# Optimization experiments

Hardware: AMD Instinct MI355X
Metric: run time of the kernel (lower is better)

Reference implementation:

```python
import jax, jax.numpy as jnp
import numpy as np

E = 8      # num_experts
K = 2      # top-k
DIM = 1024
DFF = 2048  # fused gate+up width; intermediate = DFF // 2 == DIM


def setup_inputs() -> dict:
    key = jax.random.key(0)
    ks = jax.random.split(key, 5)
    B, S = 4, 2048
    x = jax.random.normal(ks[0], (B, S, DIM), dtype=jnp.float32)
    Wg = jax.random.normal(ks[1], (E, DIM), dtype=jnp.float32) * 0.02
    bg = jax.random.normal(ks[2], (E,), dtype=jnp.float32) * 0.02
    w1 = jax.random.normal(ks[3], (E, DFF, DIM), dtype=jnp.float32) * 0.02
    w2 = jax.random.normal(ks[4], (E, DIM, DFF // 2), dtype=jnp.float32) * 0.02
    return {"x": x, "Wg": Wg, "bg": bg, "w1": w1, "w2": w2}


def _moe(x, Wg, bg, w1, w2):
    B, S, D = x.shape
    t = x.reshape(-1, D)                      # [T, D] tokens
    logits = t @ Wg.T + bg                    # [T, E]
    probs = jax.nn.softmax(logits, axis=-1)
    topw, topi = jax.lax.top_k(probs, K)      # [T, K]
    topw = topw / jnp.sum(topw, axis=-1, keepdims=True)  # renormalize=True
    # per-token combine weight for each expert (0 if not selected): [T, E]
    combine = jnp.sum(jax.nn.one_hot(topi, E, dtype=t.dtype) * topw[..., None], axis=1)

    def body(acc, packed):
        w1e, w2e, ce = packed                 # [DFF, D], [D, DFF//2], [T]
        h = t @ w1e.T                         # [T, DFF]
        gate, up = jnp.split(h, 2, axis=-1)   # silu_and_mul (SwiGLU)
        a = jax.nn.silu(gate) * up            # [T, DFF//2]
        o = a @ w2e.T                         # [T, D]
        return acc + ce[:, None] * o, None

    out, _ = jax.lax.scan(body, jnp.zeros_like(t), (w1, w2, combine.T))
    return out.reshape(B, S, D)


def reference(x, Wg, bg, w1, w2):
    return _moe(x, Wg, bg, w1, w2)
```

## Files before the change

### kernel.cpp

```cpp
#include <hip/hip_runtime.h>
#include <hip/hip_bf16.h>
#include <cstdint>

#define T_TOKENS 8192
#define DIM 1024
#define NEXP 8
#define DFFH 1024
#define ROWCAP 17408
#define NCHUNK 16

typedef __attribute__((ext_vector_type(8))) short bf16x8;
typedef __attribute__((ext_vector_type(4))) float f32x4;

__device__ __forceinline__ ushort f2bf(float f) {
  uint32_t u = __float_as_uint(f);
  uint32_t r = (u + 0x7fffu + ((u >> 16) & 1u)) >> 16;
  return (ushort)r;
}

__device__ __forceinline__ void async16(const void* g, const void* l) {
  __builtin_amdgcn_global_load_lds(
      (const __attribute__((address_space(1))) void*)(uintptr_t)g,
      (__attribute__((address_space(3))) void*)(uintptr_t)l, 16, 0, 0);
}

__global__ __launch_bounds__(256) void cast_kernel(
    const float4* __restrict__ x, const float4* __restrict__ w1,
    const float4* __restrict__ w2, ushort* __restrict__ xb,
    ushort* __restrict__ w1b, ushort* __restrict__ w2b) {
  const int NX = T_TOKENS * DIM / 4;
  const int NW1 = NEXP * 2048 * DIM / 4;
  const int NW2 = NEXP * DIM * DFFH / 4;
  const int total = NX + NW1 + NW2;
  for (int i = blockIdx.x * 256 + threadIdx.x; i < total; i += 2048 * 256) {
    float4 v; ushort* dst;
    if (i < NX) { v = x[i]; dst = xb + (size_t)i * 4; }
    else if (i < NX + NW1) { int j = i - NX; v = w1[j]; dst = w1b + (size_t)j * 4; }
    else { int j = i - NX - NW1; v = w2[j]; dst = w2b + (size_t)j * 4; }
    ushort4 o4;
    o4.x = f2bf(v.x); o4.y = f2bf(v.y); o4.z = f2bf(v.z); o4.w = f2bf(v.w);
    *(ushort4*)dst = o4;
  }
}

__global__ __launch_bounds__(256) void gate_kernel(
    const float4* __restrict__ x4, const float4* __restrict__ Wg4,
    const float* __restrict__ bg, int* __restrict__ top2e,
    float2* __restrict__ top2w) {
  __shared__ float4 wgl[NEXP * 256];
  const int tid = threadIdx.x;
  for (int i = tid; i < NEXP * 256; i += 256) wgl[i] = Wg4[i];
  __syncthreads();
  const int wave = tid >> 6, lane = tid & 63;
  const float bgsel = bg[lane & 7];
  const int t0 = (blockIdx.x * 4 + wave) * 16;
  for (int tt = 0; tt < 16; ++tt) {
    const int t = t0 + tt;
    const float4* xr = x4 + (size_t)t * 256;
    float acc[NEXP];
#pragma unroll
    for (int e = 0; e < NEXP; ++e) acc[e] = 0.f;
#pragma unroll
    for (int j = 0; j < 4; ++j) {
      float4 xv = xr[lane + j * 64];
#pragma unroll
      for (int e = 0; e < NEXP; ++e) {
        float4 wv = wgl[e * 256 + lane + j * 64];
        acc[e] += xv.x * wv.x + xv.y * wv.y + xv.z * wv.z + xv.w * wv.w;
      }
    }
#pragma unroll
    for (int e = 0; e < NEXP; ++e) {
      float v = acc[e];
      v += __shfl_xor(v, 1); v += __shfl_xor(v, 2); v += __shfl_xor(v, 4);
      acc[e] = v;
    }
    float v = acc[0];
#pragma unroll
    for (int e = 1; e < NEXP; ++e) v = ((lane & 7) == e) ? acc[e] : v;
    v += __shfl_xor(v, 8); v += __shfl_xor(v, 16); v += __shfl_xor(v, 32);
    v += bgsel;
    float m1 = v;
    m1 = fmaxf(m1, __shfl_xor(m1, 1));
    m1 = fmaxf(m1, __shfl_xor(m1, 2));
    m1 = fmaxf(m1, __shfl_xor(m1, 4));
    unsigned long long mk = __ballot(v == m1);
    int bi = (int)(__ffsll(mk) - 1) & 7;
    float v2 = (((lane & 7) == bi) ? -1e30f : v);
    float m2 = v2;
    m2 = fmaxf(m2, __shfl_xor(m2, 1));
    m2 = fmaxf(m2, __shfl_xor(m2, 2));
    m2 = fmaxf(m2, __shfl_xor(m2, 4));
    mk = __ballot(v2 == m2);
    int si = (int)(__ffsll(mk) - 1) & 7;
    if (lane == 0) {
      float w0 = 1.f / (1.f + __expf(m2 - m1));
      top2e[t] = bi | (si << 8);
      top2w[t] = make_float2(w0, 1.f - w0);
    }
  }
}

__global__ __launch_bounds__(1024) void route_kernel(
    const int* __restrict__ top2e, int* __restrict__ cnt,
    int* __restrict__ off, int* __restrict__ base ) {
  __shared__ int chunkcnt[NCHUNK][NEXP];
  const int tid = threadIdx.x;
  int c[NEXP];
#pragma unroll
  for (int e = 0; e < NEXP; ++e) c[e] = 0;
  const int4* p = (const int4*)(top2e + tid * 8);
  int4 a = p[0], b = p[1];
  int vals[8] = {a.x, a.y, a.z, a.w, b.x, b.y, b.z, b.w};
#pragma unroll
  for (int k = 0; k < 8; ++k) {
    int e0 = vals[k] & 255, e1 = (vals[k] >> 8) & 255;
#pragma unroll
    for (int e = 0; e < NEXP; ++e) c[e] += (e0 == e) + (e1 == e);
  }
#pragma unroll
  for (int e = 0; e < NEXP; ++e) {
    c[e] += __shfl_xor(c[e], 1);  c[e] += __shfl_xor(c[e], 2);
    c[e] += __shfl_xor(c[e], 4);  c[e] += __shfl_xor(c[e], 8);
    c[e] += __shfl_xor(c[e], 16); c[e] += __shfl_xor(c[e], 32);
  }
  const int wave = tid >> 6, lane = tid & 63;
  if (lane == 0) {
#pragma unroll
    for (int e = 0; e < NEXP; ++e) chunkcnt[wave][e] = c[e];
  }
  __syncthreads();
  if (tid == 0) {
    int o = 0;
    off[0] = 0;
    for (int e = 0; e < NEXP; ++e) {
      int tot = 0;
      for (int w = 0; w < NCHUNK; ++w) tot += chunkcnt[w][e];
      cnt[e] = tot;
      int run = o;
      for (int w = 0; w < NCHUNK; ++w) { base[w * NEXP + e] = run; run += chunkcnt[w][e]; }
      o += (tot + 127) & ~127;
      off[e + 1] = o;
    }
  }
}

__global__ __launch_bounds__(512) void scatter_kernel(
    const int* __restrict__ top2e, const float2* __restrict__ top2w,
    const int* __restrict__ base, int* __restrict__ rows_token,
    float* __restrict__ rows_weight) {
  __shared__ int lcnt[NEXP];
  const int tid = threadIdx.x;
  if (tid < NEXP) lcnt[tid] = 0;
  __syncthreads();
  const int b = blockIdx.x;
  const int t = b * 512 + tid;
  int pk = top2e[t];
  float2 w = top2w[t];
  int e0 = pk & 255, e1 = (pk >> 8) & 255;
  int p0 = atomicAdd(&lcnt[e0], 1);
  int p1 = atomicAdd(&lcnt[e1], 1);
  int r0 = base[b * NEXP + e0] + p0;
  int r1 = base[b * NEXP + e1] + p1;
  rows_token[r0] = t; rows_weight[r0] = w.x;
  rows_token[r1] = t; rows_weight[r1] = w.y;
}

__global__ __launch_bounds__(256) void mlpA_kernel(
    const ushort* __restrict__ xb, const ushort* __restrict__ w1b,
    const int* __restrict__ rows_token, const int* __restrict__ cnt,
    const int* __restrict__ off, ushort* __restrict__ abuf) {
  const int e = blockIdx.z, mt = blockIdx.y, nt = blockIdx.x;
  const int count = cnt[e];
  if (mt * 128 >= count) return;
  const int base = off[e];

  __shared__ ushort As[128 * 64];
  __shared__ ushort Bs[2][64 * 64];

  const int tid = threadIdx.x;
  const int wave = tid >> 6, lane = tid & 63;
  const int cg = tid & 7;
  const int r7w = (tid >> 3) & 7;
  const int cgs = (cg ^ r7w) * 8;

  const ushort* gA[4];
#pragma unroll
  for (int i = 0; i < 4; ++i) {
    int row = (i * 256 + tid) >> 3;
    int r = mt * 128 + row;
    int tok = (r < count) ? rows_token[base + r] : 0;
    gA[i] = xb + ((size_t)tok * DIM + cgs);
  }
  const ushort* gB[2][2];
#pragma unroll
  for (int i = 0; i < 2; ++i) {
    int row = (i * 256 + tid) >> 3;
    gB[0][i] = w1b + ((size_t)(e * 2048 + nt * 64 + row) * DIM + cgs);
    gB[1][i] = w1b + ((size_t)(e * 2048 + 1024 + nt * 64 + row) * DIM + cgs);
  }

  const f32x4 zero = {0.f, 0.f, 0.f, 0.f};
  f32x4 accg[2][4], accu[2][4];
#pragma unroll
  for (int m = 0; m < 2; ++m)
#pragma unroll
    for (int n = 0; n < 4; ++n) { accg[m][n] = zero; accu[m][n] = zero; }

  const int xr = (lane & 7) << 3;

  for (int k0 = 0; k0 < DIM; k0 += 64) {
#pragma unroll
    for (int i = 0; i < 4; ++i)
      async16(gA[i] + k0, &As[(i * 256 + wave * 64) * 8]);
#pragma unroll
    for (int i = 0; i < 2; ++i) {
      async16(gB[0][i] + k0, &Bs[0][(i * 256 + wave * 64) * 8]);
      async16(gB[1][i] + k0, &Bs[1][(i * 256 + wave * 64) * 8]);
    }
    __syncthreads();
#pragma unroll
    for (int kk = 0; kk < 2; ++kk) {
      const int ko = (kk * 32 + (lane >> 4) * 8) ^ xr;
      bf16x8 af0 = *(const bf16x8*)&As[(wave * 32 + (lane & 15)) * 64 + ko];
      bf16x8 af1 = *(const bf16x8*)&As[(wave * 32 + 16 + (lane & 15)) * 64 + ko];
#pragma unroll
      for (int n = 0; n < 4; ++n) {
        bf16x8 bgf = *(const bf16x8*)&Bs[0][(n * 16 + (lane & 15)) * 64 + ko];
        bf16x8 buf_ = *(const bf16x8*)&Bs[1][(n * 16 + (lane & 15)) * 64 + ko];
        accg[0][n] = __builtin_amdgcn_mfma_f32_16x16x32_bf16(af0, bgf, accg[0][n], 0, 0, 0);
        accg[1][n] = __builtin_amdgcn_mfma_f32_16x16x32_bf16(af1, bgf, accg[1][n], 0, 0, 0);
        accu[0][n] = __builtin_amdgcn_mfma_f32_16x16x32_bf16(af0, buf_, accu[0][n], 0, 0, 0);
        accu[1][n] = __builtin_amdgcn_mfma_f32_16x16x32_bf16(af1, buf_, accu[1][n], 0, 0, 0);
      }
    }
    __syncthreads();
  }

  const size_t arow0 = (size_t)(base + mt * 128 + wave * 32);
#pragma unroll
  for (int m = 0; m < 2; ++m)
#pragma unroll
    for (int n = 0; n < 4; ++n)
#pragma unroll
      for (int r = 0; r < 4; ++r) {
        float g = accg[m][n][r], u = accu[m][n][r];
        float a = (g / (1.f + __expf(-g))) * u;
        size_t row = arow0 + m * 16 + (lane >> 4) * 4 + r;
        int col = nt * 64 + n * 16 + (lane & 15);
        abuf[row * DFFH + col] = f2bf(a);
      }
}

__global__ __launch_bounds__(256) void mlpB_kernel(
    const ushort* __restrict__ abuf, const ushort* __restrict__ w2b,
    const int* __restrict__ rows_token, const float* __restrict__ rows_weight,
    const int* __restrict__ cnt, const int* __restrict__ off,
    float* __restrict__ out) {
  const int e = blockIdx.z, mt = blockIdx.y, nt = blockIdx.x;
  const int count = cnt[e];
  if (mt * 128 >= count) return;
  const int base = off[e];

  __shared__ ushort As[128 * 64];
  __shared__ ushort Bs[64 * 64];

  const int tid = threadIdx.x;
  const int wave = tid >> 6, lane = tid & 63;
  const int cg = tid & 7;
  const int r7w = (tid >> 3) & 7;
  const int cgs = (cg ^ r7w) * 8;

  const ushort* gA[4];
#pragma unroll
  for (int i = 0; i < 4; ++i) {
    int row = (i * 256 + tid) >> 3;
    gA[i] = abuf + ((size_t)(base + mt * 128 + row) * DFFH + cgs);
  }
  const ushort* gB[2];
#pragma unroll
  for (int i = 0; i < 2; ++i) {
    int row = (i * 256 + tid) >> 3;
    gB[i] = w2b + ((size_t)(e * 1024 + nt * 64 + row) * DFFH + cgs);
  }

  const f32x4 zero = {0.f, 0.f, 0.f, 0.f};
  f32x4 acc[2][4];
#pragma unroll
  for (int m = 0; m < 2; ++m)
#pragma unroll
    for (int n = 0; n < 4; ++n) acc[m][n] = zero;

  const int xr = (lane & 7) << 3;

  for (int k0 = 0; k0 < DFFH; k0 += 64) {
#pragma unroll
    for (int i = 0; i < 4; ++i)
      async16(gA[i] + k0, &As[(i * 256 + wave * 64) * 8]);
#pragma unroll
    for (int i = 0; i < 2; ++i)
      async16(gB[i] + k0, &Bs[(i * 256 + wave * 64) * 8]);
    __syncthreads();
#pragma unroll
    for (int kk = 0; kk < 2; ++kk) {
      const int ko = (kk * 32 + (lane >> 4) * 8) ^ xr;
      bf16x8 af0 = *(const bf16x8*)&As[(wave * 32 + (lane & 15)) * 64 + ko];
      bf16x8 af1 = *(const bf16x8*)&As[(wave * 32 + 16 + (lane & 15)) * 64 + ko];
#pragma unroll
      for (int n = 0; n < 4; ++n) {
        bf16x8 bf_ = *(const bf16x8*)&Bs[(n * 16 + (lane & 15)) * 64 + ko];
        acc[0][n] = __builtin_amdgcn_mfma_f32_16x16x32_bf16(af0, bf_, acc[0][n], 0, 0, 0);
        acc[1][n] = __builtin_amdgcn_mfma_f32_16x16x32_bf16(af1, bf_, acc[1][n], 0, 0, 0);
      }
    }
    __syncthreads();
  }

#pragma unroll
  for (int m = 0; m < 2; ++m) {
#pragma unroll
    for (int r = 0; r < 4; ++r) {
      int lrow = mt * 128 + wave * 32 + m * 16 + (lane >> 4) * 4 + r;
      if (lrow < count) {
        int tok = rows_token[base + lrow];
        float wgt = rows_weight[base + lrow];
#pragma unroll
        for (int n = 0; n < 4; ++n) {
          atomicAdd(&out[(size_t)tok * DIM + nt * 64 + n * 16 + (lane & 15)],
                    wgt * acc[m][n][r]);
        }
      }
    }
  }
}

extern "C" void kernel_launch(void* const* d_in, const int* in_sizes, int n_in,
                              void* d_out, int out_size, void* d_ws, size_t ws_size,
                              hipStream_t stream) {
  const float* x = (const float*)d_in[0];
  const float* Wg = (const float*)d_in[1];
  const float* bg = (const float*)d_in[2];
  const float* w1 = (const float*)d_in[3];
  const float* w2 = (const float*)d_in[4];
  float* out = (float*)d_out;

  char* ws = (char*)d_ws;
  ushort* xb = (ushort*)ws;
  ushort* w1b = xb + (size_t)T_TOKENS * DIM;
  ushort* w2b = w1b + (size_t)NEXP * 2048 * DIM;
  ushort* abuf = w2b + (size_t)NEXP * DIM * DFFH;
  char* p = (char*)(abuf + (size_t)ROWCAP * DFFH);
  int* top2e = (int*)p;            p += T_TOKENS * 4;
  float2* top2w = (float2*)p;      p += T_TOKENS * 8;
  int* rows_token = (int*)p;       p += ROWCAP * 4;
  float* rows_weight = (float*)p;  p += ROWCAP * 4;
  int* cnt = (int*)p;              p += 32;
  int* off = (int*)p;              p += 64;
  int* base = (int*)p;             p += NCHUNK * NEXP * 4;

  hipMemsetAsync(out, 0, (size_t)out_size * sizeof(float), stream);

  cast_kernel<<<2048, 256, 0, stream>>>((const float4*)x, (const float4*)w1,
                                        (const float4*)w2, xb, w1b, w2b);
  gate_kernel<<<128, 256, 0, stream>>>((const float4*)x, (const float4*)Wg, bg,
                                       top2e, top2w);
  route_kernel<<<1, 1024, 0, stream>>>(top2e, cnt, off, base);
  scatter_kernel<<<NCHUNK, 512, 0, stream>>>(top2e, top2w, base, rows_token,
                                             rows_weight);
  mlpA_kernel<<<dim3(16, 64, 8), 256, 0, stream>>>(xb, w1b, rows_token, cnt, off, abuf);
  mlpB_kernel<<<dim3(16, 64, 8), 256, 0, stream>>>(abuf, w2b, rows_token, rows_weight,
                                                   cnt, off, out);
}
```

Measured before the change: 259.8 us.

## Double-buffer LDS in expert GEMMs, use a 2x2 wave tiling, and widen mlpB N tile

Both expert GEMM kernels now double-buffer the shared-memory tiles, so the async global-to-LDS loads for the next K step are issued before the MFMAs on the current step, with one barrier per iteration. Waves are arranged 2x2, each computing a 64-row by 32- or 64-column sub-tile, which raises fragment reuse per LDS read. mlpB's N tile grows to 128 columns, halving its grid and the number of times each A tile is reloaded. The costs are double the LDS footprint, more accumulator registers, and fewer blocks in mlpB, any of which may lower occupancy.

Measured after the change: 262.2 us. About the same (+0.9%).

```diff
diff --git a/kernel.cpp b/kernel.cpp
--- a/kernel.cpp
+++ b/kernel.cpp
@@ -175,11 +175,12 @@
   if (mt * 128 >= count) return;
   const int base = off[e];
 
-  __shared__ ushort As[128 * 64];
-  __shared__ ushort Bs[2][64 * 64];
+  __shared__ ushort As[2][128 * 64];
+  __shared__ ushort Bs[2][2][64 * 64];
 
   const int tid = threadIdx.x;
   const int wave = tid >> 6, lane = tid & 63;
+  const int wm = wave >> 1, wn = wave & 1;
   const int cg = tid & 7;
   const int r7w = (tid >> 3) & 7;
   const int cgs = (cg ^ r7w) * 8;
@@ -187,67 +188,79 @@
   const ushort* gA[4];
 #pragma unroll
   for (int i = 0; i < 4; ++i) {
-    int row = (i * 256 + tid) >> 3;
+    int row = i * 32 + (tid >> 3);
     int r = mt * 128 + row;
     int tok = (r < count) ? rows_token[base + r] : 0;
     gA[i] = xb + ((size_t)tok * DIM + cgs);
   }
-  const ushort* gB[2][2];
+  const ushort* gBg[2];
+  const ushort* gBu[2];
 #pragma unroll
   for (int i = 0; i < 2; ++i) {
-    int row = (i * 256 + tid) >> 3;
-    gB[0][i] = w1b + ((size_t)(e * 2048 + nt * 64 + row) * DIM + cgs);
-    gB[1][i] = w1b + ((size_t)(e * 2048 + 1024 + nt * 64 + row) * DIM + cgs);
+    int row = i * 32 + (tid >> 3);
+    gBg[i] = w1b + ((size_t)(e * 2048 + nt * 64 + row) * DIM + cgs);
+    gBu[i] = w1b + ((size_t)(e * 2048 + 1024 + nt * 64 + row) * DIM + cgs);
+  }
+
+#define STAGE_A1(b_, k0_)                                             \
+  {                                                                   \
+    _Pragma("unroll")                                                 \
+    for (int i = 0; i < 4; ++i)                                       \
+      async16(gA[i] + (k0_), &As[b_][(i * 256 + wave * 64) * 8]);     \
+    _Pragma("unroll")                                                 \
+    for (int i = 0; i < 2; ++i) {                                     \
+      async16(gBg[i] + (k0_), &Bs[b_][0][(i * 256 + wave * 64) * 8]); \
+      async16(gBu[i] + (k0_), &Bs[b_][1][(i * 256 + wave * 64) * 8]); \
+    }                                                                 \
   }
 
   const f32x4 zero = {0.f, 0.f, 0.f, 0.f};
-  f32x4 accg[2][4], accu[2][4];
-#pragma unroll
-  for (int m = 0; m < 2; ++m)
-#pragma unroll
-    for (int n = 0; n < 4; ++n) { accg[m][n] = zero; accu[m][n] = zero; }
+  f32x4 accg[4][2], accu[4][2];
+#pragma unroll
+  for (int m = 0; m < 4; ++m)
+#pragma unroll
+    for (int n = 0; n < 2; ++n) { accg[m][n] = zero; accu[m][n] = zero; }
 
   const int xr = (lane & 7) << 3;
 
-  for (int k0 = 0; k0 < DIM; k0 += 64) {
-#pragma unroll
-    for (int i = 0; i < 4; ++i)
-      async16(gA[i] + k0, &As[(i * 256 + wave * 64) * 8]);
-#pragma unroll
-    for (int i = 0; i < 2; ++i) {
-      async16(gB[0][i] + k0, &Bs[0][(i * 256 + wave * 64) * 8]);
-      async16(gB[1][i] + k0, &Bs[1][(i * 256 + wave * 64) * 8]);
-    }
-    __syncthreads();
+  STAGE_A1(0, 0);
+  __syncthreads();
+
+  for (int t = 0; t < 16; ++t) {
+    const int b = t & 1;
+    if (t < 15) STAGE_A1(b ^ 1, (t + 1) * 64);
 #pragma unroll
     for (int kk = 0; kk < 2; ++kk) {
       const int ko = (kk * 32 + (lane >> 4) * 8) ^ xr;
-      bf16x8 af0 = *(const bf16x8*)&As[(wave * 32 + (lane & 15)) * 64 + ko];
-      bf16x8 af1 = *(const bf16x8*)&As[(wave * 32 + 16 + (lane & 15)) * 64 + ko];
-#pragma unroll
-      for (int n = 0; n < 4; ++n) {
-        bf16x8 bgf = *(const bf16x8*)&Bs[0][(n * 16 + (lane & 15)) * 64 + ko];
-        bf16x8 buf_ = *(const bf16x8*)&Bs[1][(n * 16 + (lane & 15)) * 64 + ko];
-        accg[0][n] = __builtin_amdgcn_mfma_f32_16x16x32_bf16(af0, bgf, accg[0][n], 0, 0, 0);
-        accg[1][n] = __builtin_amdgcn_mfma_f32_16x16x32_bf16(af1, bgf, accg[1][n], 0, 0, 0);
-        accu[0][n] = __builtin_amdgcn_mfma_f32_16x16x32_bf16(af0, buf_, accu[0][n], 0, 0, 0);
-        accu[1][n] = __builtin_amdgcn_mfma_f32_16x16x32_bf16(af1, buf_, accu[1][n], 0, 0, 0);
+      bf16x8 af[4];
+#pragma unroll
+      for (int m = 0; m < 4; ++m)
+        af[m] = *(const bf16x8*)&As[b][(wm * 64 + m * 16 + (lane & 15)) * 64 + ko];
+#pragma unroll
+      for (int n = 0; n < 2; ++n) {
+        bf16x8 bgf = *(const bf16x8*)&Bs[b][0][(wn * 32 + n * 16 + (lane & 15)) * 64 + ko];
+        bf16x8 buf_ = *(const bf16x8*)&Bs[b][1][(wn * 32 + n * 16 + (lane & 15)) * 64 + ko];
+#pragma unroll
+        for (int m = 0; m < 4; ++m) {
+          accg[m][n] = __builtin_amdgcn_mfma_f32_16x16x32_bf16(af[m], bgf, accg[m][n], 0, 0, 0);
+          accu[m][n] = __builtin_amdgcn_mfma_f32_16x16x32_bf16(af[m], buf_, accu[m][n], 0, 0, 0);
+        }
       }
     }
     __syncthreads();
   }
 
-  const size_t arow0 = (size_t)(base + mt * 128 + wave * 32);
-#pragma unroll
-  for (int m = 0; m < 2; ++m)
-#pragma unroll
-    for (int n = 0; n < 4; ++n)
+  const size_t arow0 = (size_t)(base + mt * 128 + wm * 64);
+#pragma unroll
+  for (int m = 0; m < 4; ++m)
+#pragma unroll
+    for (int n = 0; n < 2; ++n)
 #pragma unroll
       for (int r = 0; r < 4; ++r) {
         float g = accg[m][n][r], u = accu[m][n][r];
         float a = (g / (1.f + __expf(-g))) * u;
         size_t row = arow0 + m * 16 + (lane >> 4) * 4 + r;
-        int col = nt * 64 + n * 16 + (lane & 15);
+        int col = nt * 64 + wn * 32 + n * 16 + (lane & 15);
         abuf[row * DFFH + col] = f2bf(a);
       }
 }
@@ -262,11 +275,12 @@
   if (mt * 128 >= count) return;
   const int base = off[e];
 
-  __shared__ ushort As[128 * 64];
-  __shared__ ushort Bs[64 * 64];
+  __shared__ ushort As[2][128 * 64];
+  __shared__ ushort Bs[2][128 * 64];
 
   const int tid = threadIdx.x;
   const int wave = tid >> 6, lane = tid & 63;
+  const int wm = wave >> 1, wn = wave & 1;
   const int cg = tid & 7;
   const int r7w = (tid >> 3) & 7;
   const int cgs = (cg ^ r7w) * 8;
@@ -274,59 +288,69 @@
   const ushort* gA[4];
 #pragma unroll
   for (int i = 0; i < 4; ++i) {
-    int row = (i * 256 + tid) >> 3;
+    int row = i * 32 + (tid >> 3);
     gA[i] = abuf + ((size_t)(base + mt * 128 + row) * DFFH + cgs);
   }
-  const ushort* gB[2];
-#pragma unroll
-  for (int i = 0; i < 2; ++i) {
-    int row = (i * 256 + tid) >> 3;
-    gB[i] = w2b + ((size_t)(e * 1024 + nt * 64 + row) * DFFH + cgs);
+  const ushort* gB[4];
+#pragma unroll
+  for (int i = 0; i < 4; ++i) {
+    int row = i * 32 + (tid >> 3);
+    gB[i] = w2b + ((size_t)(e * 1024 + nt * 128 + row) * DFFH + cgs);
+  }
+
+#define STAGE_B1(b_, k0_)                                           \
+  {                                                                 \
+    _Pragma("unroll")                                               \
+    for (int i = 0; i < 4; ++i) {                                   \
+      async16(gA[i] + (k0_), &As[b_][(i * 256 + wave * 64) * 8]);   \
+      async16(gB[i] + (k0_), &Bs[b_][(i * 256 + wave * 64) * 8]);   \
+    }                                                               \
   }
 
   const f32x4 zero = {0.f, 0.f, 0.f, 0.f};
-  f32x4 acc[2][4];
-#pragma unroll
-  for (int m = 0; m < 2; ++m)
+  f32x4 acc[4][4];
+#pragma unroll
+  for (int m = 0; m < 4; ++m)
 #pragma unroll
     for (int n = 0; n < 4; ++n) acc[m][n] = zero;
 
   const int xr = (lane & 7) << 3;
 
-  for (int k0 = 0; k0 < DFFH; k0 += 64) {
-#pragma unroll
-    for (int i = 0; i < 4; ++i)
-      async16(gA[i] + k0, &As[(i * 256 + wave * 64) * 8]);
-#pragma unroll
-    for (int i = 0; i < 2; ++i)
-      async16(gB[i] + k0, &Bs[(i * 256 + wave * 64) * 8]);
-    __syncthreads();
+  STAGE_B1(0, 0);
+  __syncthreads();
+
+  for (int t = 0; t < 16; ++t) {
+    const int b = t & 1;
+    if (t < 15) STAGE_B1(b ^ 1, (t + 1) * 64);
 #pragma unroll
     for (int kk = 0; kk < 2; ++kk) {
       const int ko = (kk * 32 + (lane >> 4) * 8) ^ xr;
-      bf16x8 af0 = *(const bf16x8*)&As[(wave * 32 + (lane & 15)) * 64 + ko];
-      bf16x8 af1 = *(const bf16x8*)&As[(wave * 32 + 16 + (lane & 15)) * 64 + ko];
+      bf16x8 af[4];
+#pragma unroll
+      for (int m = 0; m < 4; ++m)
+        af[m] = *(const bf16x8*)&As[b][(wm * 64 + m * 16 + (lane & 15)) * 64 + ko];
 #pragma unroll
       for (int n = 0; n < 4; ++n) {
-        bf16x8 bf_ = *(const bf16x8*)&Bs[(n * 16 + (lane & 15)) * 64 + ko];
-        acc[0][n] = __builtin_amdgcn_mfma_f32_16x16x32_bf16(af0, bf_, acc[0][n], 0, 0, 0);
-        acc[1][n] = __builtin_amdgcn_mfma_f32_16x16x32_bf16(af1, bf_, acc[1][n], 0, 0, 0);
+        bf16x8 bf_ = *(const bf16x8*)&Bs[b][(wn * 64 + n * 16 + (lane & 15)) * 64 + ko];
+#pragma unroll
+        for (int m = 0; m < 4; ++m)
+          acc[m][n] = __builtin_amdgcn_mfma_f32_16x16x32_bf16(af[m], bf_, acc[m][n], 0, 0, 0);
       }
     }
     __syncthreads();
   }
 
 #pragma unroll
-  for (int m = 0; m < 2; ++m) {
+  for (int m = 0; m < 4; ++m) {
 #pragma unroll
     for (int r = 0; r < 4; ++r) {
-      int lrow = mt * 128 + wave * 32 + m * 16 + (lane >> 4) * 4 + r;
+      int lrow = mt * 128 + wm * 64 + m * 16 + (lane >> 4) * 4 + r;
       if (lrow < count) {
         int tok = rows_token[base + lrow];
         float wgt = rows_weight[base + lrow];
 #pragma unroll
         for (int n = 0; n < 4; ++n) {
-          atomicAdd(&out[(size_t)tok * DIM + nt * 64 + n * 16 + (lane & 15)],
+          atomicAdd(&out[(size_t)tok * DIM + nt * 128 + wn * 64 + n * 16 + (lane & 15)],
                     wgt * acc[m][n][r]);
         }
       }
@@ -368,6 +392,6 @@
   scatter_kernel<<<NCHUNK, 512, 0, stream>>>(top2e, top2w, base, rows_token,
                                              rows_weight);
   mlpA_kernel<<<dim3(16, 64, 8), 256, 0, stream>>>(xb, w1b, rows_token, cnt, off, abuf);
-  mlpB_kernel<<<dim3(16, 64, 8), 256, 0, stream>>>(abuf, w2b, rows_token, rows_weight,
-                                                   cnt, off, out);
-}
+  mlpB_kernel<<<dim3(8, 64, 8), 256, 0, stream>>>(abuf, w2b, rows_token, rows_weight,
+                                                  cnt, off, out);
+}
```
